# Kernel tuning notes

Measured on AMD Instinct MI355X. Metric: run time of the kernel, lower is better.

Reference implementation:

```python
import jax, jax.numpy as jnp
import numpy as np

D_IN = 1024
D_OUT = 1024
NUM_HEADS = 16
HEAD_DIM = D_OUT // NUM_HEADS


def setup_inputs() -> dict:
    key = jax.random.key(0)
    k_x, k_qkv, k_pw, k_pb = jax.random.split(key, 4)
    x = jax.random.normal(k_x, (2, 2048, D_IN), dtype=jnp.float32)
    # torch nn.Linear(d_in, 3*d_out, bias=False): weight [3*d_out, d_in]
    w_qkv = jax.random.normal(k_qkv, (3 * D_OUT, D_IN), dtype=jnp.float32) * (1.0 / np.sqrt(D_IN))
    # proj: nn.Linear(d_out, d_out) with bias
    w_proj = jax.random.normal(k_pw, (D_OUT, D_OUT), dtype=jnp.float32) * (1.0 / np.sqrt(D_OUT))
    b_proj = jax.random.normal(k_pb, (D_OUT,), dtype=jnp.float32) * 0.01
    return {"x": x, "w_qkv": w_qkv, "w_proj": w_proj, "b_proj": b_proj}


def reference(x, w_qkv, w_proj, b_proj):
    B, S, _ = x.shape
    # fused QKV projection: [B,S,3*D_OUT]
    qkv = jnp.einsum('bsd,ed->bse', x, w_qkv)
    qkv = qkv.reshape(B, S, 3, NUM_HEADS, HEAD_DIM)
    q, k, v = jnp.moveaxis(qkv, 2, 0)  # each [B,S,H,Dh]
    scale = 1.0 / jnp.sqrt(jnp.asarray(HEAD_DIM, dtype=x.dtype))
    # scores [B,H,S,S]
    scores = jnp.einsum('bqhd,bkhd->bhqk', q, k) * scale
    causal = jnp.tril(jnp.ones((S, S), dtype=bool))
    scores = jnp.where(causal, scores, jnp.asarray(-jnp.inf, dtype=scores.dtype))
    attn = jax.nn.softmax(scores, axis=-1)
    ctx = jnp.einsum('bhqk,bkhd->bqhd', attn, v)  # [B,S,H,Dh]
    ctx = ctx.reshape(B, S, D_OUT)
    return jnp.einsum('bsd,ed->bse', ctx, w_proj) + b_proj
```

## Files before the change

kernel.cpp:

```cpp
#include <hip/hip_runtime.h>
#include <hip/hip_bf16.h>
#include <cstdint>

#define B_SZ   2
#define S_LEN  2048
#define NH     16
#define NT     32
#define LDA    72

using f32x4 = __attribute__((ext_vector_type(4))) float;
typedef __bf16 bf16x8 __attribute__((ext_vector_type(8)));
typedef __bf16 bf16x4 __attribute__((ext_vector_type(4)));

__device__ inline float bf2f(unsigned short u) {
    union { unsigned int i; float f; } v; v.i = ((unsigned int)u) << 16; return v.f;
}
__device__ inline unsigned short f2bf(float f) {
    union { float f; unsigned int i; } v; v.f = f;
    unsigned int r = v.i + 0x7fff + ((v.i >> 16) & 1);
    return (unsigned short)(r >> 16);
}
__device__ inline f32x4 mfma16(bf16x8 a, bf16x8 b, f32x4 c) {
    return __builtin_amdgcn_mfma_f32_16x16x32_bf16(a, b, c, 0, 0, 0);
}
__device__ inline unsigned pack_bf16x2(float lo, float hi) {
    float2 f2; f2.x = lo; f2.y = hi;
    __hip_bfloat162 bb = __float22bfloat162_rn(f2);
    union { __hip_bfloat162 b; unsigned u; } cv; cv.b = bb;
    return cv.u;
}
__device__ inline void stC(float* C, size_t idx, float v)  { C[idx] = v; }
__device__ inline void stC(__bf16* C, size_t idx, float v) { ((unsigned short*)C)[idx] = f2bf(v); }

__global__ __launch_bounds__(256) void f2b2_kernel(
    const float* __restrict__ a, int na4, __bf16* __restrict__ outa,
    const float* __restrict__ b, int nb4, __bf16* __restrict__ outb)
{
    int i = blockIdx.x * blockDim.x + threadIdx.x;
    const float* src; __bf16* dst; int idx;
    if (i < na4)           { src = a; dst = outa; idx = i; }
    else if (i < na4 + nb4){ src = b; dst = outb; idx = i - na4; }
    else return;
    float4 v = ((const float4*)src)[idx];
    ushort4 o;
    o.x = f2bf(v.x); o.y = f2bf(v.y); o.z = f2bf(v.z); o.w = f2bf(v.w);
    ((ushort4*)dst)[idx] = o;
}

__global__ __launch_bounds__(256) void f2b_kernel(
    const float* __restrict__ in, __bf16* __restrict__ out, int n4)
{
    int i = blockIdx.x * blockDim.x + threadIdx.x;
    if (i < n4) {
        float4 v = ((const float4*)in)[i];
        ushort4 o;
        o.x = f2bf(v.x); o.y = f2bf(v.y); o.z = f2bf(v.z); o.w = f2bf(v.w);
        ((ushort4*)out)[i] = o;
    }
}

template <typename TO, int HAS_BIAS>
__global__ __launch_bounds__(256) void gemm128(
    const __bf16* __restrict__ A, const __bf16* __restrict__ W,
    const float* __restrict__ bias, TO* __restrict__ C,
    int M, int N, int K)
{
    __shared__ __bf16 Alds[2][128 * 32];
    __shared__ __bf16 Blds[2][128 * 32];
    const int tid  = threadIdx.x, lane = tid & 63, w = tid >> 6;
    const int c16  = lane & 15, quad = lane >> 4;
    const int mBase = blockIdx.y * 128, nBase = blockIdx.x * 128;
    const int moff = (w & 1) * 64, noff = (w >> 1) * 64;

    f32x4 acc[4][4];
#pragma unroll
    for (int i = 0; i < 4; ++i)
#pragma unroll
        for (int j = 0; j < 4; ++j) acc[i][j] = (f32x4){0.f, 0.f, 0.f, 0.f};

    auto stage = [&](int buf, int k0) {
#pragma unroll
        for (int p = 0; p < 2; ++p) {
            const int linear = p * 256 + tid;
            const int row = linear >> 2;
            const int seg = (linear & 3) ^ (row & 3);
            const int lbase = (p * 256 + w * 64) * 8;
            const __bf16* ga = A + (size_t)(mBase + row) * K + k0 + seg * 8;
            const __bf16* gb = W + (size_t)(nBase + row) * K + k0 + seg * 8;
            __builtin_amdgcn_global_load_lds(
                (const __attribute__((address_space(1))) void*)ga,
                (__attribute__((address_space(3))) void*)(&Alds[buf][lbase]), 16, 0, 0);
            __builtin_amdgcn_global_load_lds(
                (const __attribute__((address_space(1))) void*)gb,
                (__attribute__((address_space(3))) void*)(&Blds[buf][lbase]), 16, 0, 0);
        }
    };

    stage(0, 0);
    int cur = 0;
    for (int k0 = 0; k0 < K; k0 += 32) {
        __syncthreads();
        if (k0 + 32 < K) stage(cur ^ 1, k0 + 32);

        bf16x8 af[4], bw[4];
#pragma unroll
        for (int i = 0; i < 4; ++i) {
            const int rowA = moff + i * 16 + c16;
            af[i] = *(const bf16x8*)&Alds[cur][rowA * 32 + ((quad ^ (rowA & 3)) << 3)];
            const int rowB = noff + i * 16 + c16;
            bw[i] = *(const bf16x8*)&Blds[cur][rowB * 32 + ((quad ^ (rowB & 3)) << 3)];
        }
#pragma unroll
        for (int i = 0; i < 4; ++i)
#pragma unroll
            for (int j = 0; j < 4; ++j)
                acc[i][j] = mfma16(af[i], bw[j], acc[i][j]);
        cur ^= 1;
    }

#pragma unroll
    for (int j = 0; j < 4; ++j) {
        const int col = nBase + noff + j * 16 + c16;
        const float bv = HAS_BIAS ? bias[col] : 0.f;
#pragma unroll
        for (int i = 0; i < 4; ++i)
#pragma unroll
            for (int r = 0; r < 4; ++r) {
                const int row = mBase + moff + i * 16 + quad * 4 + r;
                stC(C, (size_t)row * N + col, acc[i][j][r] + bv);
            }
    }
}

template <typename TO, int HAS_BIAS>
__global__ __launch_bounds__(256) void gemm64(
    const __bf16* __restrict__ A, const __bf16* __restrict__ W,
    const float* __restrict__ bias, TO* __restrict__ C,
    int M, int N, int K)
{
    __shared__ __bf16 Alds[2][64 * 32];
    __shared__ __bf16 Blds[2][128 * 32];
    const int tid  = threadIdx.x, lane = tid & 63, w = tid >> 6;
    const int c16  = lane & 15, quad = lane >> 4;
    const int mBase = blockIdx.y * 64, nBase = blockIdx.x * 128;
    const int moff = (w & 1) * 32, noff = (w >> 1) * 64;

    f32x4 acc[2][4];
#pragma unroll
    for (int i = 0; i < 2; ++i)
#pragma unroll
        for (int j = 0; j < 4; ++j) acc[i][j] = (f32x4){0.f, 0.f, 0.f, 0.f};

    auto stage = [&](int buf, int k0) {
        {
            const int row = tid >> 2;
            const int seg = (tid & 3) ^ (row & 3);
            const int lbase = (w * 64) * 8;
            const __bf16* ga = A + (size_t)(mBase + row) * K + k0 + seg * 8;
            __builtin_amdgcn_global_load_lds(
                (const __attribute__((address_space(1))) void*)ga,
                (__attribute__((address_space(3))) void*)(&Alds[buf][lbase]), 16, 0, 0);
        }
#pragma unroll
        for (int p = 0; p < 2; ++p) {
            const int linear = p * 256 + tid;
            const int row = linear >> 2;
            const int seg = (linear & 3) ^ (row & 3);
            const int lbase = (p * 256 + w * 64) * 8;
            const __bf16* gb = W + (size_t)(nBase + row) * K + k0 + seg * 8;
            __builtin_amdgcn_global_load_lds(
                (const __attribute__((address_space(1))) void*)gb,
                (__attribute__((address_space(3))) void*)(&Blds[buf][lbase]), 16, 0, 0);
        }
    };

    stage(0, 0);
    int cur = 0;
    for (int k0 = 0; k0 < K; k0 += 32) {
        __syncthreads();
        if (k0 + 32 < K) stage(cur ^ 1, k0 + 32);

        bf16x8 af[2], bw[4];
#pragma unroll
        for (int i = 0; i < 2; ++i) {
            const int rowA = moff + i * 16 + c16;
            af[i] = *(const bf16x8*)&Alds[cur][rowA * 32 + ((quad ^ (rowA & 3)) << 3)];
        }
#pragma unroll
        for (int j = 0; j < 4; ++j) {
            const int rowB = noff + j * 16 + c16;
            bw[j] = *(const bf16x8*)&Blds[cur][rowB * 32 + ((quad ^ (rowB & 3)) << 3)];
        }
#pragma unroll
        for (int i = 0; i < 2; ++i)
#pragma unroll
            for (int j = 0; j < 4; ++j)
                acc[i][j] = mfma16(af[i], bw[j], acc[i][j]);
        cur ^= 1;
    }

#pragma unroll
    for (int j = 0; j < 4; ++j) {
        const int col = nBase + noff + j * 16 + c16;
        const float bv = HAS_BIAS ? bias[col] : 0.f;
#pragma unroll
        for (int i = 0; i < 2; ++i)
#pragma unroll
            for (int r = 0; r < 4; ++r) {
                const int row = mBase + moff + i * 16 + quad * 4 + r;
                stC(C, (size_t)row * N + col, acc[i][j][r] + bv);
            }
    }
}

__global__ __launch_bounds__(256) void attn(
    const __bf16* __restrict__ qkv, __bf16* __restrict__ ctx,
    float* __restrict__ opart, float* __restrict__ lpart)
{
    __shared__ __bf16 Qs[64 * LDA];
    __shared__ __bf16 Ks[64 * LDA];
    __shared__ __bf16 Vs[64 * LDA];

    const int tid  = threadIdx.x;
    const int lane = tid & 63;
    const int w    = tid >> 6;
    const int c16  = lane & 15;
    const int quad = lane >> 4;
    const int bh = blockIdx.x, b = bh >> 4, h = bh & 15;
    const int y  = blockIdx.y;

    int qt, c0, c1, seg;
    bool split;
    if (y < 16)      { qt = 16 + y; const int half = (qt + 2) >> 1; c0 = 0;    c1 = half;   split = true;  seg = 0; }
    else if (y < 32) { qt = y;      const int half = (qt + 2) >> 1; c0 = half; c1 = qt + 1; split = true;  seg = 1; }
    else             { qt = 47 - y; c0 = 0; c1 = qt + 1; split = false; seg = 0; }
    const int qBase = qt * 64;
    const int segIdx = split ? ((bh * 16 + (qt - 16)) * 2 + seg) : 0;

    const float QS = 0.125f * 1.4426950408889634f;

    const int krow0 = tid >> 3;
    const int kd0   = (tid & 7) * 8;
    const int c16t = tid & 15;
    const int jh   = (tid >> 4) & 1;
    const int dblk = tid >> 5;

    const size_t rowB = (size_t)b * S_LEN;
    const __bf16* kp0 = qkv + (rowB + c0 * 64 + krow0) * 3072 + 1024 + h * 64 + kd0;
    const __bf16* kp1 = kp0 + (size_t)32 * 3072;
    const __bf16* vp0 = qkv + (rowB + c0 * 64 + 2 * jh * 16 + c16t) * 3072 + 2048 + h * 64 + dblk * 8;
    const __bf16* vp1 = vp0 + (size_t)16 * 3072;

    uint4 kr0 = *(const uint4*)kp0;
    uint4 kr1 = *(const uint4*)kp1;
    uint4 vr0 = *(const uint4*)vp0;
    uint4 vr1 = *(const uint4*)vp1;

#pragma unroll
    for (int p = 0; p < 2; ++p) {
        const int linear = p * 256 + tid;
        const int row = linear >> 3;
        const int d0 = (linear & 7) * 8;
        const __bf16* g = qkv + (rowB + qBase + row) * 3072 + h * 64 + d0;
        uint4 raw = *(const uint4*)g;
        const unsigned short* u = (const unsigned short*)&raw;
        unsigned short tmp[8];
#pragma unroll
        for (int jj = 0; jj < 8; ++jj) tmp[jj] = f2bf(bf2f(u[jj]) * QS);
        *(uint4*)&Qs[row * LDA + d0] = *(const uint4*)tmp;
    }
    __syncthreads();

    const bf16x8 aq0 = *(const bf16x8*)&Qs[(w * 16 + c16) * LDA + quad * 8];
    const bf16x8 aq1 = *(const bf16x8*)&Qs[(w * 16 + c16) * LDA + 32 + quad * 8];

    float lp = 0.f;
    f32x4 acc_o[4];
#pragma unroll
    for (int j = 0; j < 4; ++j) acc_o[j] = (f32x4){0.f, 0.f, 0.f, 0.f};

    for (int cc = c0; cc < c1; ++cc) {
        *(uint4*)&Ks[krow0 * LDA + kd0]        = kr0;
        *(uint4*)&Ks[(krow0 + 32) * LDA + kd0] = kr1;
        {
            const unsigned short* e1 = (const unsigned short*)&vr0;
            const unsigned short* e2 = (const unsigned short*)&vr1;
#pragma unroll
            for (int d = 0; d < 8; ++d) {
                const unsigned pack = (unsigned)e1[d] | ((unsigned)e2[d] << 16);
                *(unsigned*)&Vs[(dblk * 8 + d) * LDA + c16t * 4 + 2 * jh] = pack;
            }
        }
        __syncthreads();

        if (cc + 1 < c1) {
            kp0 += (size_t)64 * 3072; kp1 += (size_t)64 * 3072;
            vp0 += (size_t)64 * 3072; vp1 += (size_t)64 * 3072;
            kr0 = *(const uint4*)kp0;
            kr1 = *(const uint4*)kp1;
            vr0 = *(const uint4*)vp0;
            vr1 = *(const uint4*)vp1;
        }

        f32x4 sc[4];
#pragma unroll
        for (int j = 0; j < 4; ++j) sc[j] = (f32x4){0.f, 0.f, 0.f, 0.f};
#pragma unroll
        for (int j = 0; j < 4; ++j) {
            bf16x8 bk0 = *(const bf16x8*)&Ks[(j * 16 + c16) * LDA + quad * 8];
            bf16x8 bk1 = *(const bf16x8*)&Ks[(j * 16 + c16) * LDA + 32 + quad * 8];
            sc[j] = mfma16(bk0, aq0, sc[j]);
            sc[j] = mfma16(bk1, aq1, sc[j]);
        }

        if (cc == qt) {
            const int q = qBase + w * 16 + c16;
#pragma unroll
            for (int j = 0; j < 4; ++j) {
#pragma unroll
                for (int r = 0; r < 4; ++r) {
                    const int key = cc * 64 + j * 16 + quad * 4 + r;
                    if (key > q) sc[j][r] = -1e30f;
                }
            }
        }

        float p_[4][4];
#pragma unroll
        for (int j = 0; j < 4; ++j)
#pragma unroll
            for (int r = 0; r < 4; ++r)
                p_[j][r] = exp2f(sc[j][r]);
#pragma unroll
        for (int j = 0; j < 4; ++j)
            lp += (p_[j][0] + p_[j][1]) + (p_[j][2] + p_[j][3]);

        unsigned Wp[2][4];
#pragma unroll
        for (int r = 0; r < 4; ++r) {
            Wp[0][r] = pack_bf16x2(p_[0][r], p_[1][r]);
            Wp[1][r] = pack_bf16x2(p_[2][r], p_[3][r]);
        }

        const int q0 = quad & 1, q1 = quad >> 1;
        const int src0 = 16 * q1 + c16;
        const int src1 = 32 + 16 * q1 + c16;
        unsigned a0w[4], a1w[4];
#pragma unroll
        for (int t = 0; t < 4; ++t) {
            const int j2 = t & 1, rb = t >> 1;
            unsigned lo0 = (unsigned)__shfl((int)Wp[j2][rb],     src0);
            unsigned hi0 = (unsigned)__shfl((int)Wp[j2][2 + rb], src0);
            a0w[t] = q0 ? hi0 : lo0;
            unsigned lo1 = (unsigned)__shfl((int)Wp[j2][rb],     src1);
            unsigned hi1 = (unsigned)__shfl((int)Wp[j2][2 + rb], src1);
            a1w[t] = q0 ? hi1 : lo1;
        }
        union { unsigned u[4]; bf16x8 v; } U0, U1;
#pragma unroll
        for (int t = 0; t < 4; ++t) { U0.u[t] = a0w[t]; U1.u[t] = a1w[t]; }
        const bf16x8 ap0 = U0.v;
        const bf16x8 ap1 = U1.v;

#pragma unroll
        for (int j = 0; j < 4; ++j) {
            bf16x8 bv0 = *(const bf16x8*)&Vs[(j * 16 + c16) * LDA + quad * 8];
            bf16x8 bv1 = *(const bf16x8*)&Vs[(j * 16 + c16) * LDA + 32 + quad * 8];
            acc_o[j] = mfma16(ap0, bv0, acc_o[j]);
            acc_o[j] = mfma16(ap1, bv1, acc_o[j]);
        }
        __syncthreads();
    }

    lp += __shfl_xor(lp, 16);
    lp += __shfl_xor(lp, 32);

    if (!split) {
#pragma unroll
        for (int r = 0; r < 4; ++r) {
            const float inv = 1.0f / __shfl(lp, quad * 4 + r);
            const size_t rowO = (rowB + qBase + w * 16 + quad * 4 + r) * 1024 + h * 64;
#pragma unroll
            for (int j = 0; j < 4; ++j)
                ctx[rowO + j * 16 + c16] = (__bf16)(acc_o[j][r] * inv);
        }
    } else {
        float* ob = opart + (size_t)segIdx * 4096;
        if (quad == 0) lpart[segIdx * 64 + w * 16 + c16] = lp;
#pragma unroll
        for (int r = 0; r < 4; ++r) {
            const int qrow = w * 16 + quad * 4 + r;
#pragma unroll
            for (int j = 0; j < 4; ++j)
                ob[qrow * 64 + j * 16 + c16] = acc_o[j][r];
        }
    }
}

__global__ __launch_bounds__(256) void attn_combine(
    const float* __restrict__ opart, const float* __restrict__ lpart,
    __bf16* __restrict__ ctx)
{
    const int blk = blockIdx.x;
    const int bh = blk >> 4, t = blk & 15;
    const int b = bh >> 4, h = bh & 15;
    const int qt = 16 + t;
    const int tid = threadIdx.x;
    const int q  = tid >> 2;
    const int d0 = (tid & 3) * 16;
    const int segA = blk * 2, segB = segA + 1;
    const float* oa = opart + (size_t)segA * 4096 + q * 64 + d0;
    const float* obp = opart + (size_t)segB * 4096 + q * 64 + d0;
    const float inv = 1.0f / (lpart[segA * 64 + q] + lpart[segB * 64 + q]);
    unsigned short outv[16];
#pragma unroll
    for (int i = 0; i < 4; ++i) {
        float4 a = ((const float4*)oa)[i];
        float4 c = ((const float4*)obp)[i];
        outv[4 * i + 0] = f2bf((a.x + c.x) * inv);
        outv[4 * i + 1] = f2bf((a.y + c.y) * inv);
        outv[4 * i + 2] = f2bf((a.z + c.z) * inv);
        outv[4 * i + 3] = f2bf((a.w + c.w) * inv);
    }
    __bf16* dst = ctx + ((size_t)(b * S_LEN + qt * 64 + q)) * 1024 + h * 64 + d0;
    *(uint4*)dst       = *(const uint4*)&outv[0];
    *(uint4*)(dst + 8) = *(const uint4*)&outv[8];
}

extern "C" void kernel_launch(void* const* d_in, const int* in_sizes, int n_in,
                              void* d_out, int out_size, void* d_ws, size_t ws_size,
                              hipStream_t stream) {
    const float* x      = (const float*)d_in[0];
    const float* w_qkv  = (const float*)d_in[1];
    const float* w_proj = (const float*)d_in[2];
    const float* b_proj = (const float*)d_in[3];
    float* out = (float*)d_out;

    __bf16* qkvb = (__bf16*)d_ws;
    __bf16* xb   = qkvb + (size_t)4096 * 3072;
    __bf16* wqb  = xb + (size_t)4096 * 1024;
    __bf16* ctxb = xb;
    __bf16* wpb  = wqb;
    float*  lpart = (float*)(wqb + (size_t)1024 * 1024);
    float* opart = out;

    const int M = B_SZ * S_LEN;
    const int nx4 = 4096 * 1024 / 4, nq4 = 3072 * 1024 / 4, np4 = 1024 * 1024 / 4;

    f2b2_kernel<<<(nx4 + nq4 + 255) / 256, 256, 0, stream>>>(x, nx4, xb, w_qkv, nq4, wqb);

    gemm128<__bf16, 0><<<dim3(3072 / 128, M / 128), 256, 0, stream>>>(
        xb, wqb, nullptr, qkvb, M, 3072, 1024);

    f2b_kernel<<<(np4 + 255) / 256, 256, 0, stream>>>(w_proj, wpb, np4);

    attn<<<dim3(B_SZ * NH, 48), 256, 0, stream>>>(qkvb, ctxb, opart, lpart);
    attn_combine<<<B_SZ * NH * 16, 256, 0, stream>>>(opart, lpart, ctxb);

    gemm64<float, 1><<<dim3(1024 / 128, M / 64), 256, 0, stream>>>(
        ctxb, wpb, b_proj, out, M, 1024, 1024);
}
```

Before: 191.1 us.

## Compute transposed PV product to eliminate cross-lane shuffles of probabilities

Reorders the PV MFMA so V (from LDS) is the A operand and the packed probabilities are the B operand. The P fragment then comes straight from each lane's own softmax registers, with no __shfl. The V LDS store layout is permuted to match, and the output then comes out transposed per lane. This allows vectorized bf16x4 and f32x4 stores for ctx and the partial outputs, and drops the per-row lp shuffle. The aim is to remove the 16 shuffles per tile and the scalar stores, at the cost of a more intricate V staging permutation that could cause LDS bank conflicts.

After: 185.9 us. 1.03x faster.

```diff
diff --git a/kernel.cpp b/kernel.cpp
--- a/kernel.cpp
+++ b/kernel.cpp
@@ -241,15 +241,15 @@
 
     const int krow0 = tid >> 3;
     const int kd0   = (tid & 7) * 8;
-    const int c16t = tid & 15;
-    const int jh   = (tid >> 4) & 1;
-    const int dblk = tid >> 5;
+    const int u     = tid & 31;
+    const int dblk  = tid >> 5;
+    const int vcol  = 32 * (u & 1) + 8 * ((u >> 1) & 3) + 2 * (u >> 3);
 
     const size_t rowB = (size_t)b * S_LEN;
     const __bf16* kp0 = qkv + (rowB + c0 * 64 + krow0) * 3072 + 1024 + h * 64 + kd0;
     const __bf16* kp1 = kp0 + (size_t)32 * 3072;
-    const __bf16* vp0 = qkv + (rowB + c0 * 64 + 2 * jh * 16 + c16t) * 3072 + 2048 + h * 64 + dblk * 8;
-    const __bf16* vp1 = vp0 + (size_t)16 * 3072;
+    const __bf16* vp0 = qkv + (rowB + c0 * 64 + 2 * u) * 3072 + 2048 + h * 64 + dblk * 8;
+    const __bf16* vp1 = vp0 + (size_t)3072;
 
     uint4 kr0 = *(const uint4*)kp0;
     uint4 kr1 = *(const uint4*)kp1;
@@ -263,10 +263,10 @@
         const int d0 = (linear & 7) * 8;
         const __bf16* g = qkv + (rowB + qBase + row) * 3072 + h * 64 + d0;
         uint4 raw = *(const uint4*)g;
-        const unsigned short* u = (const unsigned short*)&raw;
+        const unsigned short* uu = (const unsigned short*)&raw;
         unsigned short tmp[8];
 #pragma unroll
-        for (int jj = 0; jj < 8; ++jj) tmp[jj] = f2bf(bf2f(u[jj]) * QS);
+        for (int jj = 0; jj < 8; ++jj) tmp[jj] = f2bf(bf2f(uu[jj]) * QS);
         *(uint4*)&Qs[row * LDA + d0] = *(const uint4*)tmp;
     }
     __syncthreads();
@@ -288,7 +288,7 @@
 #pragma unroll
             for (int d = 0; d < 8; ++d) {
                 const unsigned pack = (unsigned)e1[d] | ((unsigned)e2[d] << 16);
-                *(unsigned*)&Vs[(dblk * 8 + d) * LDA + c16t * 4 + 2 * jh] = pack;
+                *(unsigned*)&Vs[(dblk * 8 + d) * LDA + vcol] = pack;
             }
         }
         __syncthreads();
@@ -335,39 +335,21 @@
         for (int j = 0; j < 4; ++j)
             lp += (p_[j][0] + p_[j][1]) + (p_[j][2] + p_[j][3]);
 
-        unsigned Wp[2][4];
-#pragma unroll
-        for (int r = 0; r < 4; ++r) {
-            Wp[0][r] = pack_bf16x2(p_[0][r], p_[1][r]);
-            Wp[1][r] = pack_bf16x2(p_[2][r], p_[3][r]);
-        }
-
-        const int q0 = quad & 1, q1 = quad >> 1;
-        const int src0 = 16 * q1 + c16;
-        const int src1 = 32 + 16 * q1 + c16;
-        unsigned a0w[4], a1w[4];
-#pragma unroll
-        for (int t = 0; t < 4; ++t) {
-            const int j2 = t & 1, rb = t >> 1;
-            unsigned lo0 = (unsigned)__shfl((int)Wp[j2][rb],     src0);
-            unsigned hi0 = (unsigned)__shfl((int)Wp[j2][2 + rb], src0);
-            a0w[t] = q0 ? hi0 : lo0;
-            unsigned lo1 = (unsigned)__shfl((int)Wp[j2][rb],     src1);
-            unsigned hi1 = (unsigned)__shfl((int)Wp[j2][2 + rb], src1);
-            a1w[t] = q0 ? hi1 : lo1;
-        }
-        union { unsigned u[4]; bf16x8 v; } U0, U1;
-#pragma unroll
-        for (int t = 0; t < 4; ++t) { U0.u[t] = a0w[t]; U1.u[t] = a1w[t]; }
-        const bf16x8 ap0 = U0.v;
-        const bf16x8 ap1 = U1.v;
-
+        union { unsigned uu[4]; bf16x8 v; } B0, B1;
 #pragma unroll
         for (int j = 0; j < 4; ++j) {
-            bf16x8 bv0 = *(const bf16x8*)&Vs[(j * 16 + c16) * LDA + quad * 8];
-            bf16x8 bv1 = *(const bf16x8*)&Vs[(j * 16 + c16) * LDA + 32 + quad * 8];
-            acc_o[j] = mfma16(ap0, bv0, acc_o[j]);
-            acc_o[j] = mfma16(ap1, bv1, acc_o[j]);
+            B0.uu[j] = pack_bf16x2(p_[j][0], p_[j][1]);
+            B1.uu[j] = pack_bf16x2(p_[j][2], p_[j][3]);
+        }
+        const bf16x8 bp0 = B0.v;
+        const bf16x8 bp1 = B1.v;
+
+#pragma unroll
+        for (int jd = 0; jd < 4; ++jd) {
+            bf16x8 av0 = *(const bf16x8*)&Vs[(jd * 16 + c16) * LDA + quad * 8];
+            bf16x8 av1 = *(const bf16x8*)&Vs[(jd * 16 + c16) * LDA + 32 + quad * 8];
+            acc_o[jd] = mfma16(av0, bp0, acc_o[jd]);
+            acc_o[jd] = mfma16(av1, bp1, acc_o[jd]);
         }
         __syncthreads();
     }
@@ -376,24 +358,21 @@
     lp += __shfl_xor(lp, 32);
 
     if (!split) {
-#pragma unroll
-        for (int r = 0; r < 4; ++r) {
-            const float inv = 1.0f / __shfl(lp, quad * 4 + r);
-            const size_t rowO = (rowB + qBase + w * 16 + quad * 4 + r) * 1024 + h * 64;
-#pragma unroll
-            for (int j = 0; j < 4; ++j)
-                ctx[rowO + j * 16 + c16] = (__bf16)(acc_o[j][r] * inv);
+        const float inv = 1.0f / lp;
+        const size_t rowO = (rowB + qBase + w * 16 + c16) * 1024 + h * 64;
+#pragma unroll
+        for (int jd = 0; jd < 4; ++jd) {
+            bf16x4 ov;
+#pragma unroll
+            for (int r = 0; r < 4; ++r) ov[r] = (__bf16)(acc_o[jd][r] * inv);
+            *(bf16x4*)&ctx[rowO + jd * 16 + quad * 4] = ov;
         }
     } else {
-        float* ob = opart + (size_t)segIdx * 4096;
+        float* ob = opart + (size_t)segIdx * 4096 + (w * 16 + c16) * 64;
         if (quad == 0) lpart[segIdx * 64 + w * 16 + c16] = lp;
 #pragma unroll
-        for (int r = 0; r < 4; ++r) {
-            const int qrow = w * 16 + quad * 4 + r;
-#pragma unroll
-            for (int j = 0; j < 4; ++j)
-                ob[qrow * 64 + j * 16 + c16] = acc_o[j][r];
-        }
+        for (int jd = 0; jd < 4; ++jd)
+            *(f32x4*)&ob[jd * 16 + quad * 4] = acc_o[jd];
     }
 }
 
```
